# Optimization experiments

Measured on AMD Instinct MI355X. Metric: run time of the kernel, lower is better.

## Reference

```python
import jax, jax.numpy as jnp
import numpy as np

D_MODEL = 1024
N_HEADS = 16
HEAD_DIM = D_MODEL // N_HEADS
D_FF = 4 * D_MODEL
LN_EPS = 1e-5


def setup_inputs() -> dict:
    key = jax.random.key(0)
    ks = jax.random.split(key, 12)
    B, T = 16, 512
    s = lambda fan_in: 1.0 / np.sqrt(fan_in)
    inp = {
        'x': jax.random.normal(ks[0], (B, T, D_MODEL), jnp.float32),
        # torch Linear layout: [out_features, in_features]
        'w_qkv': jax.random.normal(ks[1], (3 * D_MODEL, D_MODEL), jnp.float32) * s(D_MODEL),
        'w_proj': jax.random.normal(ks[2], (D_MODEL, D_MODEL), jnp.float32) * s(D_MODEL),
        'w_ff1': jax.random.normal(ks[3], (D_FF, D_MODEL), jnp.float32) * s(D_MODEL),
        'b_ff1': jax.random.normal(ks[4], (D_FF,), jnp.float32) * 0.02,
        'w_ff2': jax.random.normal(ks[5], (D_MODEL, D_FF), jnp.float32) * s(D_FF),
        'b_ff2': jax.random.normal(ks[6], (D_MODEL,), jnp.float32) * 0.02,
        'ln1_g': jnp.ones((D_MODEL,), jnp.float32),
        'ln1_b': jnp.zeros((D_MODEL,), jnp.float32),
        'ln2_g': jnp.ones((D_MODEL,), jnp.float32),
        'ln2_b': jnp.zeros((D_MODEL,), jnp.float32),
    }
    return inp


def _layernorm(x, g, b):
    mu = jnp.mean(x, axis=-1, keepdims=True)
    var = jnp.var(x, axis=-1, keepdims=True)
    return (x - mu) * jax.lax.rsqrt(var + LN_EPS) * g + b


def _block(x, w_qkv, w_proj, w_ff1, b_ff1, w_ff2, b_ff2, ln1_g, ln1_b, ln2_g, ln2_b):
    B, T, _ = x.shape
    a = _layernorm(x, ln1_g, ln1_b)
    qkv = a @ w_qkv.T  # [B,T,3D]
    q, k, v = jnp.split(qkv, 3, axis=-1)
    # [B,H,T,hd]
    rs = lambda t: t.reshape(B, T, N_HEADS, HEAD_DIM).transpose(0, 2, 1, 3)
    q, k, v = rs(q), rs(k), rs(v)
    scale = HEAD_DIM ** -0.5
    att = jnp.einsum('bhqd,bhkd->bhqk', q, k) * scale
    causal = jnp.tril(jnp.ones((T, T), bool))
    att = jnp.where(causal, att, jnp.float32(-10000.0))
    att = jax.nn.softmax(att, axis=-1)
    out = jnp.einsum('bhqk,bhkd->bhqd', att, v)
    out = out.transpose(0, 2, 1, 3).reshape(B, T, D_MODEL)
    x = x + out @ w_proj.T
    f = _layernorm(x, ln2_g, ln2_b)
    f = jax.nn.gelu(f @ w_ff1.T + b_ff1, approximate=False) @ w_ff2.T + b_ff2
    return x + f


def reference(x, w_qkv, w_proj, w_ff1, b_ff1, w_ff2, b_ff2, ln1_g, ln1_b, ln2_g, ln2_b):
    return _block(x, w_qkv, w_proj, w_ff1, b_ff1, w_ff2, b_ff2, ln1_g, ln1_b, ln2_g, ln2_b)
```

## Files before the change

kernel.cpp:

```cpp
#include <hip/hip_runtime.h>
#include <stdint.h>

typedef __bf16 bf16x8_t __attribute__((ext_vector_type(8)));
typedef float f32x4_t __attribute__((ext_vector_type(4)));

#define DEV __device__ __forceinline__

DEV unsigned short f2bf(float f) {
  union { float f; uint32_t u; } v; v.f = f;
  uint32_t r = v.u + 0x7FFFu + ((v.u >> 16) & 1u);
  return (unsigned short)(r >> 16);
}

DEV void gl_lds16(const void* g, void* l) {
  __builtin_amdgcn_global_load_lds(
      (const __attribute__((address_space(1))) void*)g,
      (__attribute__((address_space(3))) void*)l, 16, 0, 0);
}

DEV void barx() {
  asm volatile("" ::: "memory");
  __builtin_amdgcn_s_barrier();
  asm volatile("" ::: "memory");
}

#define VMC(N) asm volatile("s_waitcnt vmcnt(" #N ")" ::: "memory")

DEV float gelu_f(float x) {
  const float y = x * 0.7071067811865475f;
  const float ay = fabsf(y);
  const float t = __builtin_amdgcn_rcpf(1.0f + 0.3275911f * ay);
  float p = fmaf(t, 1.061405429f, -1.453152027f);
  p = fmaf(t, p, 1.421413741f);
  p = fmaf(t, p, -0.284496736f);
  p = fmaf(t, p, 0.254829592f);
  p *= t;
  const float e = __expf(-ay * ay);
  float erfv = 1.0f - p * e;
  erfv = copysignf(erfv, y);
  return 0.5f * x * (1.0f + erfv);
}

__global__ __launch_bounds__(256) void cvt_all(const float* __restrict__ w0, unsigned short* __restrict__ o0,
                                               const float* __restrict__ w1, unsigned short* __restrict__ o1,
                                               const float* __restrict__ w2, unsigned short* __restrict__ o2,
                                               const float* __restrict__ w3, unsigned short* __restrict__ o3) {
  int i = blockIdx.x * 256 + threadIdx.x;
  const float* in; unsigned short* outp;
  if (i < 786432) { in = w0; outp = o0; }
  else if (i < 1048576) { in = w1; outp = o1; i -= 786432; }
  else if (i < 2097152) { in = w2; outp = o2; i -= 1048576; }
  else { in = w3; outp = o3; i -= 2097152; }
  float4 v = ((const float4*)in)[i];
  ushort4 o;
  o.x = f2bf(v.x); o.y = f2bf(v.y); o.z = f2bf(v.z); o.w = f2bf(v.w);
  ((ushort4*)outp)[i] = o;
}

__global__ __launch_bounds__(256) void ln_kernel(const float* __restrict__ x,
                                                 const float* __restrict__ g,
                                                 const float* __restrict__ b,
                                                 unsigned short* __restrict__ outp) {
  const int row = blockIdx.x * 4 + (threadIdx.x >> 6);
  const int lane = threadIdx.x & 63;
  const float4* xr = (const float4*)(x + (size_t)row * 1024);
  float4 v[4];
  float s = 0.f, s2 = 0.f;
#pragma unroll
  for (int j = 0; j < 4; ++j) {
    v[j] = xr[j * 64 + lane];
    s += v[j].x + v[j].y + v[j].z + v[j].w;
    s2 += v[j].x * v[j].x + v[j].y * v[j].y + v[j].z * v[j].z + v[j].w * v[j].w;
  }
#pragma unroll
  for (int off = 1; off < 64; off <<= 1) {
    s += __shfl_xor(s, off, 64);
    s2 += __shfl_xor(s2, off, 64);
  }
  const float mu = s * (1.0f / 1024.0f);
  const float var = s2 * (1.0f / 1024.0f) - mu * mu;
  const float rstd = rsqrtf(var + 1e-5f);
  ushort4* orow = (ushort4*)(outp + (size_t)row * 1024);
  const float4* gp = (const float4*)g;
  const float4* bp = (const float4*)b;
#pragma unroll
  for (int j = 0; j < 4; ++j) {
    float4 gv = gp[j * 64 + lane], bv = bp[j * 64 + lane];
    ushort4 o;
    o.x = f2bf((v[j].x - mu) * rstd * gv.x + bv.x);
    o.y = f2bf((v[j].y - mu) * rstd * gv.y + bv.y);
    o.z = f2bf((v[j].z - mu) * rstd * gv.z + bv.z);
    o.w = f2bf((v[j].w - mu) * rstd * gv.w + bv.w);
    orow[j * 64 + lane] = o;
  }
}


#define RD_AF(DST, BUF, MH, PC)                                               \
  _Pragma("unroll") for (int mi = 0; mi < 4; ++mi)                            \
      DST[mi] = *(const bf16x8_t*)((BUF) + (wm + (MH)*64 + mi * 16 + l16) * 64 + (PC));

#define RD_BF(DST, BUF, PC)                                                   \
  _Pragma("unroll") for (int ni = 0; ni < 4; ++ni)                            \
      DST[ni] = *(const bf16x8_t*)((BUF) + (wn + ni * 16 + l16) * 64 + (PC));

#define MFMA16(MH, AA, BB)                                                    \
  __builtin_amdgcn_s_setprio(1);                                              \
  _Pragma("unroll") for (int mi = 0; mi < 4; ++mi)                            \
  _Pragma("unroll") for (int ni = 0; ni < 4; ++ni)                            \
      acc[(MH)*4 + mi][ni] = __builtin_amdgcn_mfma_f32_16x16x32_bf16(         \
          AA[mi], BB[ni], acc[(MH)*4 + mi][ni], 0, 0, 0);                     \
  __builtin_amdgcn_s_setprio(0);

#define DMA_A(BUF, Q, KT) gl_lds16(aBase + (size_t)((Q)*64) * lda + (size_t)(KT)*64, &sA[BUF][(Q)*4096 + sdo])
#define DMA_B(BUF, Q, KT) gl_lds16(bBase + (size_t)((Q)*64) * lda + (size_t)(KT)*64, &sB[BUF][(Q)*4096 + sdo])

#define TILE(T, CB, B0c, B1c, B0n)                                            \
  {                                                                           \
    const int t1 = ((T) + 1 < nt) ? (T) + 1 : nt - 1;                         \
    const int t2 = ((T) + 2 < nt) ? (T) + 2 : nt - 1;                         \
    const unsigned short* pA = &sA[CB][0];                                    \
    const unsigned short* pB = &sB[CB][0];                                    \
                                                                     \
    barx(); VMC(8);                                                           \
    RD_AF(aO, pA, 0, pc1) RD_BF(B1c, pB, pc1)                                 \
    MFMA16(0, aE, B0c)                                                        \
    DMA_A(CB ^ 1, 1, t1); DMA_A(CB ^ 1, 3, t1);                               \
                                                                     \
    barx(); VMC(8);                                                           \
    RD_AF(aE, pA, 1, pc0)                                                     \
    MFMA16(0, aO, B1c)                                                        \
    DMA_B(CB, 0, t2); DMA_B(CB, 1, t2);                                       \
                                                                     \
    barx();                                                                   \
    RD_AF(aO, pA, 1, pc1)                                                     \
    MFMA16(1, aE, B0c)                                                        \
    DMA_A(CB, 0, t2); DMA_A(CB, 2, t2);                                       \
                                                                     \
    barx(); VMC(6);                                                           \
    RD_AF(aE, &sA[CB ^ 1][0], 0, pc0) RD_BF(B0n, &sB[CB ^ 1][0], pc0)         \
    MFMA16(1, aO, B1c)                                                        \
    DMA_B(CB, 2, t2); DMA_B(CB, 3, t2);                                       \
  }

template <int MODE>
__global__ __launch_bounds__(512) void gemm8(const unsigned short* __restrict__ A,
                                             const unsigned short* __restrict__ B,
                                             float* __restrict__ Cf,
                                             unsigned short* __restrict__ Cb,
                                             const float* __restrict__ bias,
                                             const float* __restrict__ res,
                                             unsigned short* __restrict__ Vt,
                                             int M, int N, int K, int lda) {
  __shared__ unsigned short sA[2][256 * 64];
  __shared__ unsigned short sB[2][256 * 64];
  const int tid = threadIdx.x;
  const int w = tid >> 6, lane = tid & 63;
  const int kg = lane >> 4, l16 = lane & 15;
  const int wm = (w & 1) * 128, wn = (w >> 1) * 64;

  const int nwg = gridDim.x;
  const int bid = blockIdx.x;
  const int cid = (bid & 7) * (nwg >> 3) + (bid >> 3);
  int ks = 0, cc = cid;
  if (MODE == 4) { ks = cid >> 7; cc = cid & 127; }
  const int rowBase = (cc & 31) * 256;
  const int colBase = (cc >> 5) * 256;
  const int koff = ks * K;

  const int srow = tid >> 3, sch = tid & 7;
  const unsigned short* aBase = A + (size_t)(rowBase + srow) * lda + koff + ((sch ^ (srow & 7)) * 8);
  const unsigned short* bBase = B + (size_t)(colBase + srow) * lda + koff + ((sch ^ (srow & 7)) * 8);
  const int sdo = tid * 8;

  f32x4_t acc[8][4];
#pragma unroll
  for (int mi = 0; mi < 8; ++mi)
#pragma unroll
    for (int ni = 0; ni < 4; ++ni) acc[mi][ni] = (f32x4_t)0.0f;

  const int nt = K >> 6;
  const int pc0 = ((kg ^ (l16 & 7)) & 7) * 8;
  const int pc1 = (((4 + kg) ^ (l16 & 7)) & 7) * 8;

  bf16x8_t aE[4], aO[4], B0a[4], B1a[4], B0b[4], B1b[4];

  {
    const int t1p = 1 < nt ? 1 : 0;
#pragma unroll
    for (int q = 0; q < 4; ++q) DMA_A(0, q, 0);
#pragma unroll
    for (int q = 0; q < 4; ++q) DMA_B(0, q, 0);
    DMA_A(1, 0, t1p); DMA_A(1, 2, t1p);
#pragma unroll
    for (int q = 0; q < 4; ++q) DMA_B(1, q, t1p);
  }
  VMC(6);
  barx();
  RD_AF(aE, &sA[0][0], 0, pc0)
  RD_BF(B0a, &sB[0][0], pc0)

  for (int t = 0; t < nt; t += 2) {
    TILE(t, 0, B0a, B1a, B0b)
    TILE(t + 1, 1, B0b, B1b, B0a)
  }

#pragma unroll
  for (int mi = 0; mi < 8; ++mi) {
#pragma unroll
    for (int ni = 0; ni < 4; ++ni) {
      const int col = colBase + wn + ni * 16 + l16;
      if (MODE == 0 && colBase >= 2048) {
        const int c2 = col - 2048;
        const int hh = c2 >> 6, dd = c2 & 63;
        const int rw = rowBase + wm + mi * 16 + kg * 4;
        ushort4 pk;
        pk.x = f2bf(acc[mi][ni][0]);
        pk.y = f2bf(acc[mi][ni][1]);
        pk.z = f2bf(acc[mi][ni][2]);
        pk.w = f2bf(acc[mi][ni][3]);
        *(ushort4*)(Vt + (((size_t)(rw >> 9) * 16 + hh) * 64 + dd) * 512 + (rw & 511)) = pk;
        continue;
      }
      float bv = 0.f;
      if (MODE == 2 || MODE == 3 || (MODE == 4 && ks == 0)) bv = bias[col];
#pragma unroll
      for (int r = 0; r < 4; ++r) {
        const int row = rowBase + wm + mi * 16 + kg * 4 + r;
        const size_t idx = (size_t)row * N + col;
        float v = acc[mi][ni][r];
        if (MODE == 0) {
          Cb[idx] = f2bf(v);
        } else if (MODE == 1) {
          Cf[idx] = v + res[idx];
        } else if (MODE == 2) {
          Cb[idx] = f2bf(gelu_f(v + bv));
        } else if (MODE == 3) {
          Cf[idx] = v + bv + res[idx];
        } else {
          if (ks == 0) {
            Cf[idx] = v + bv + res[idx];
          } else {
            float* P = (rowBase < 4096) ? (float*)Cb : (float*)Vt;
            P[(size_t)((row & 4095)) * N + col] = v;
          }
        }
      }
    }
  }
  asm volatile("s_waitcnt vmcnt(0)" ::: "memory");
}

__global__ __launch_bounds__(256) void ff2_fin(float* __restrict__ outp,
                                               const float* __restrict__ p1a,
                                               const float* __restrict__ p1b) {
  const int i = blockIdx.x * 256 + threadIdx.x;
  float4 v = ((float4*)outp)[i];
  const float4 p = (i < 1048576) ? ((const float4*)p1a)[i] : ((const float4*)p1b)[i - 1048576];
  v.x += p.x; v.y += p.y; v.z += p.z; v.w += p.w;
  ((float4*)outp)[i] = v;
}

__global__ __launch_bounds__(256) void attn_kernel(const unsigned short* __restrict__ qkv,
                                                   const unsigned short* __restrict__ Vt,
                                                   unsigned short* __restrict__ outp) {
  constexpr int D3 = 3072;
  __shared__ unsigned short sQ[128 * 64];
  __shared__ unsigned short sK[64 * 64];
  __shared__ unsigned short sVt[64 * 64];
  __shared__ unsigned short sP[128 * 72];
  const int tid = threadIdx.x;
  const int w = tid >> 6, lane = tid & 63;
  const int kg = lane >> 4, l16 = lane & 15;
  const int qi = (int)gridDim.x - 1 - (int)blockIdx.x;
  const int h = blockIdx.y, bb = blockIdx.z;
  const int t0 = qi * 128;
  const size_t base = (size_t)bb * 512 * D3 + h * 64;

  const int sr = tid >> 3;
  const int sc = ((tid & 7) ^ (sr & 7)) * 8;

  {
    const unsigned short* g = qkv + base + (size_t)(t0 + sr) * D3 + sc;
    unsigned short* l = sQ + tid * 8;
#pragma unroll
    for (int i = 0; i < 4; ++i) gl_lds16(g + (size_t)32 * i * D3, l + 2048 * i);
  }

  const unsigned short* gVbase = Vt + ((size_t)(bb * 16 + h) * 64 + sr) * 512 + sc;

  bf16x8_t ones;
#pragma unroll
  for (int j = 0; j < 8; ++j) ones[j] = (__bf16)1.0f;

  const int wm = w * 32;
  f32x4_t o[2][4];
  f32x4_t lsum[2];
#pragma unroll
  for (int mi = 0; mi < 2; ++mi) {
    lsum[mi] = (f32x4_t)0.0f;
#pragma unroll
    for (int di = 0; di < 4; ++di) o[mi][di] = (f32x4_t)0.0f;
  }

  const int nkt = (qi + 1) * 2;
  for (int kt = 0; kt < nkt; ++kt) {
    const int k0 = kt * 64;
    __syncthreads();
    {
      const unsigned short* g = qkv + base + 1024 + (size_t)(k0 + sr) * D3 + sc;
      unsigned short* l = sK + tid * 8;
      gl_lds16(g, l);
      gl_lds16(g + (size_t)32 * D3, l + 2048);
    }
    {
      const unsigned short* g = gVbase + k0;
      unsigned short* l = sVt + tid * 8;
      gl_lds16(g, l);
      gl_lds16(g + (size_t)32 * 512, l + 2048);
    }
    __syncthreads();

    const bool active = (k0 <= t0 + wm + 31);
    if (active) {
      f32x4_t s[2][4];
#pragma unroll
      for (int mi = 0; mi < 2; ++mi)
#pragma unroll
        for (int ni = 0; ni < 4; ++ni) s[mi][ni] = (f32x4_t)0.0f;
#pragma unroll
      for (int kd = 0; kd < 2; ++kd) {
        bf16x8_t aq[2], bk[4];
#pragma unroll
        for (int mi = 0; mi < 2; ++mi) {
          const int rr = wm + mi * 16 + l16;
          aq[mi] = *(const bf16x8_t*)(sQ + rr * 64 + (((kd * 4 + kg) ^ (l16 & 7)) * 8));
        }
#pragma unroll
        for (int ni = 0; ni < 4; ++ni) {
          const int rr = ni * 16 + l16;
          bk[ni] = *(const bf16x8_t*)(sK + rr * 64 + (((kd * 4 + kg) ^ (l16 & 7)) * 8));
        }
#pragma unroll
        for (int mi = 0; mi < 2; ++mi)
#pragma unroll
          for (int ni = 0; ni < 4; ++ni)
            s[mi][ni] = __builtin_amdgcn_mfma_f32_16x16x32_bf16(aq[mi], bk[ni], s[mi][ni], 0, 0, 0);
      }
#pragma unroll
      for (int mi = 0; mi < 2; ++mi) {
#pragma unroll
        for (int r = 0; r < 4; ++r) {
          const int q = t0 + wm + mi * 16 + kg * 4 + r;
          const int prow = wm + mi * 16 + kg * 4 + r;
#pragma unroll
          for (int ni = 0; ni < 4; ++ni) {
            const int kk = k0 + ni * 16 + l16;
            const float p = (kk <= q) ? __expf(s[mi][ni][r] * 0.125f) : 0.0f;
            sP[prow * 72 + ni * 16 + l16] = f2bf(p);
          }
        }
      }
#pragma unroll
      for (int kd = 0; kd < 2; ++kd) {
        bf16x8_t ap[2], bv[4];
#pragma unroll
        for (int mi = 0; mi < 2; ++mi)
          ap[mi] = *(const bf16x8_t*)(sP + (wm + mi * 16 + l16) * 72 + kd * 32 + kg * 8);
#pragma unroll
        for (int di = 0; di < 4; ++di) {
          const int dd = di * 16 + l16;
          bv[di] = *(const bf16x8_t*)(sVt + dd * 64 + (((kd * 4 + kg) ^ (l16 & 7)) * 8));
        }
#pragma unroll
        for (int mi = 0; mi < 2; ++mi) {
#pragma unroll
          for (int di = 0; di < 4; ++di)
            o[mi][di] = __builtin_amdgcn_mfma_f32_16x16x32_bf16(ap[mi], bv[di], o[mi][di], 0, 0, 0);
          lsum[mi] = __builtin_amdgcn_mfma_f32_16x16x32_bf16(ap[mi], ones, lsum[mi], 0, 0, 0);
        }
      }
    }
  }

#pragma unroll
  for (int mi = 0; mi < 2; ++mi) {
#pragma unroll
    for (int r = 0; r < 4; ++r) {
      const float inv = 1.0f / lsum[mi][r];
      const int row = t0 + wm + mi * 16 + kg * 4 + r;
      const size_t ob = ((size_t)bb * 512 + row) * 1024 + h * 64;
#pragma unroll
      for (int di = 0; di < 4; ++di)
        outp[ob + di * 16 + l16] = f2bf(o[mi][di][r] * inv);
    }
  }
}

extern "C" void kernel_launch(void* const* d_in, const int* in_sizes, int n_in,
                              void* d_out, int out_size, void* d_ws, size_t ws_size,
                              hipStream_t stream) {
  const float* x      = (const float*)d_in[0];
  const float* w_qkv  = (const float*)d_in[1];
  const float* w_proj = (const float*)d_in[2];
  const float* w_ff1  = (const float*)d_in[3];
  const float* b_ff1  = (const float*)d_in[4];
  const float* w_ff2  = (const float*)d_in[5];
  const float* b_ff2  = (const float*)d_in[6];
  const float* ln1_g  = (const float*)d_in[7];
  const float* ln1_b  = (const float*)d_in[8];
  const float* ln2_g  = (const float*)d_in[9];
  const float* ln2_b  = (const float*)d_in[10];
  float* out = (float*)d_out;
  char* ws = (char*)d_ws;

  unsigned short* wqkv_b  = (unsigned short*)(ws + 0);
  unsigned short* wproj_b = (unsigned short*)(ws + 6291456);
  unsigned short* wff1_b  = (unsigned short*)(ws + 8388608);
  unsigned short* wff2_b  = (unsigned short*)(ws + 16777216);
  unsigned short* a_b     = (unsigned short*)(ws + 25165824);
  float*          x2_f    = (float*)(ws + 41943040);
  unsigned short* vt_b    = (unsigned short*)(ws + 41943040);
  unsigned short* qkv_b   = (unsigned short*)(ws + 75497472);
  unsigned short* attn_b  = (unsigned short*)(ws + 125829120);
  unsigned short* h_b     = qkv_b;
  float* p1a = (float*)a_b;
  float* p1b = (float*)attn_b;

  cvt_all<<<12288, 256, 0, stream>>>(w_qkv, wqkv_b, w_proj, wproj_b, w_ff1, wff1_b, w_ff2, wff2_b);

  ln_kernel<<<2048, 256, 0, stream>>>(x, ln1_g, ln1_b, a_b);
  gemm8<0><<<384, 512, 0, stream>>>(a_b, wqkv_b, nullptr, qkv_b, nullptr, nullptr, vt_b, 8192, 3072, 1024, 1024);
  attn_kernel<<<dim3(4, 16, 16), 256, 0, stream>>>(qkv_b, vt_b, attn_b);
  gemm8<1><<<128, 512, 0, stream>>>(attn_b, wproj_b, x2_f, nullptr, nullptr, x, nullptr, 8192, 1024, 1024, 1024);
  ln_kernel<<<2048, 256, 0, stream>>>(x2_f, ln2_g, ln2_b, a_b);
  gemm8<2><<<512, 512, 0, stream>>>(a_b, wff1_b, nullptr, h_b, b_ff1, nullptr, nullptr, 8192, 4096, 1024, 1024);
  gemm8<4><<<256, 512, 0, stream>>>(h_b, wff2_b, out, (unsigned short*)p1a, b_ff2, x2_f, (unsigned short*)p1b, 8192, 1024, 2048, 4096);
  ff2_fin<<<8192, 256, 0, stream>>>(out, p1a, p1b);
}
```

Measured before the change: 484.9 us.

## Restructure GEMM main loop into per-k-tile four-phase schedule with simpler buffering

Replaces the two-tile unrolled TILE macro pipeline, which prefetched A/B fragments into registers across tiles, with a single k-tile loop split into four phases. Each phase reads a 32-row A slice plus the full B fragment set from LDS, issues part of the next tile's DMA, waits on lgkmcnt, and runs the MFMAs. Register pressure and fragment ping-ponging drop, but there are more barriers and no LDS-read/MFMA overlap across phases, since each phase waits with lgkmcnt(0) before its MFMAs.

Measured after the change: 525.4 us. +8.4%, slower.

```diff
diff --git a/kernel.cpp b/kernel.cpp
--- a/kernel.cpp
+++ b/kernel.cpp
@@ -25,6 +25,11 @@
 }
 
 #define VMC(N) asm volatile("s_waitcnt vmcnt(" #N ")" ::: "memory")
+#define LGKM(N) asm volatile("s_waitcnt lgkmcnt(" #N ")" ::: "memory")
+
+DEV f32x4_t mfma(bf16x8_t a, bf16x8_t b, f32x4_t c) {
+  return __builtin_amdgcn_mfma_f32_16x16x32_bf16(a, b, c, 0, 0, 0);
+}
 
 DEV float gelu_f(float x) {
   const float y = x * 0.7071067811865475f;
@@ -96,52 +101,30 @@
 }
 
 
-#define RD_AF(DST, BUF, MH, PC)                                               \
-  _Pragma("unroll") for (int mi = 0; mi < 4; ++mi)                            \
-      DST[mi] = *(const bf16x8_t*)((BUF) + (wm + (MH)*64 + mi * 16 + l16) * 64 + (PC));
-
-#define RD_BF(DST, BUF, PC)                                                   \
-  _Pragma("unroll") for (int ni = 0; ni < 4; ++ni)                            \
-      DST[ni] = *(const bf16x8_t*)((BUF) + (wn + ni * 16 + l16) * 64 + (PC));
-
-#define MFMA16(MH, AA, BB)                                                    \
+#define RD_A4(Q, BUF)                                                         \
+  aF[0] = *(const bf16x8_t*)((BUF) + (wm + (Q)*32 + l16) * 64 + pc0);         \
+  aF[1] = *(const bf16x8_t*)((BUF) + (wm + (Q)*32 + l16) * 64 + pc1);         \
+  aF[2] = *(const bf16x8_t*)((BUF) + (wm + (Q)*32 + 16 + l16) * 64 + pc0);    \
+  aF[3] = *(const bf16x8_t*)((BUF) + (wm + (Q)*32 + 16 + l16) * 64 + pc1);
+
+#define RD_B8(BUF)                                                            \
+  _Pragma("unroll") for (int ni = 0; ni < 4; ++ni) {                          \
+    bF[ni] = *(const bf16x8_t*)((BUF) + (wn + ni * 16 + l16) * 64 + pc0);     \
+    bF[4 + ni] = *(const bf16x8_t*)((BUF) + (wn + ni * 16 + l16) * 64 + pc1); \
+  }
+
+#define MFMA_Q(Q)                                                             \
   __builtin_amdgcn_s_setprio(1);                                              \
-  _Pragma("unroll") for (int mi = 0; mi < 4; ++mi)                            \
-  _Pragma("unroll") for (int ni = 0; ni < 4; ++ni)                            \
-      acc[(MH)*4 + mi][ni] = __builtin_amdgcn_mfma_f32_16x16x32_bf16(         \
-          AA[mi], BB[ni], acc[(MH)*4 + mi][ni], 0, 0, 0);                     \
+  _Pragma("unroll") for (int ni = 0; ni < 4; ++ni) {                          \
+    acc[(Q)*2][ni] = mfma(aF[0], bF[ni], acc[(Q)*2][ni]);                     \
+    acc[(Q)*2][ni] = mfma(aF[1], bF[4 + ni], acc[(Q)*2][ni]);                 \
+    acc[(Q)*2 + 1][ni] = mfma(aF[2], bF[ni], acc[(Q)*2 + 1][ni]);             \
+    acc[(Q)*2 + 1][ni] = mfma(aF[3], bF[4 + ni], acc[(Q)*2 + 1][ni]);         \
+  }                                                                           \
   __builtin_amdgcn_s_setprio(0);
 
 #define DMA_A(BUF, Q, KT) gl_lds16(aBase + (size_t)((Q)*64) * lda + (size_t)(KT)*64, &sA[BUF][(Q)*4096 + sdo])
 #define DMA_B(BUF, Q, KT) gl_lds16(bBase + (size_t)((Q)*64) * lda + (size_t)(KT)*64, &sB[BUF][(Q)*4096 + sdo])
-
-#define TILE(T, CB, B0c, B1c, B0n)                                            \
-  {                                                                           \
-    const int t1 = ((T) + 1 < nt) ? (T) + 1 : nt - 1;                         \
-    const int t2 = ((T) + 2 < nt) ? (T) + 2 : nt - 1;                         \
-    const unsigned short* pA = &sA[CB][0];                                    \
-    const unsigned short* pB = &sB[CB][0];                                    \
-                                                                     \
-    barx(); VMC(8);                                                           \
-    RD_AF(aO, pA, 0, pc1) RD_BF(B1c, pB, pc1)                                 \
-    MFMA16(0, aE, B0c)                                                        \
-    DMA_A(CB ^ 1, 1, t1); DMA_A(CB ^ 1, 3, t1);                               \
-                                                                     \
-    barx(); VMC(8);                                                           \
-    RD_AF(aE, pA, 1, pc0)                                                     \
-    MFMA16(0, aO, B1c)                                                        \
-    DMA_B(CB, 0, t2); DMA_B(CB, 1, t2);                                       \
-                                                                     \
-    barx();                                                                   \
-    RD_AF(aO, pA, 1, pc1)                                                     \
-    MFMA16(1, aE, B0c)                                                        \
-    DMA_A(CB, 0, t2); DMA_A(CB, 2, t2);                                       \
-                                                                     \
-    barx(); VMC(6);                                                           \
-    RD_AF(aE, &sA[CB ^ 1][0], 0, pc0) RD_BF(B0n, &sB[CB ^ 1][0], pc0)         \
-    MFMA16(1, aO, B1c)                                                        \
-    DMA_B(CB, 2, t2); DMA_B(CB, 3, t2);                                       \
-  }
 
 template <int MODE>
 __global__ __launch_bounds__(512) void gemm8(const unsigned short* __restrict__ A,
@@ -183,26 +166,51 @@
   const int pc0 = ((kg ^ (l16 & 7)) & 7) * 8;
   const int pc1 = (((4 + kg) ^ (l16 & 7)) & 7) * 8;
 
-  bf16x8_t aE[4], aO[4], B0a[4], B1a[4], B0b[4], B1b[4];
-
-  {
-    const int t1p = 1 < nt ? 1 : 0;
-#pragma unroll
-    for (int q = 0; q < 4; ++q) DMA_A(0, q, 0);
-#pragma unroll
-    for (int q = 0; q < 4; ++q) DMA_B(0, q, 0);
-    DMA_A(1, 0, t1p); DMA_A(1, 2, t1p);
-#pragma unroll
-    for (int q = 0; q < 4; ++q) DMA_B(1, q, t1p);
-  }
-  VMC(6);
+  DMA_A(0, 0, 0); DMA_A(0, 2, 0);
+  DMA_B(0, 0, 0); DMA_B(0, 1, 0); DMA_B(0, 2, 0); DMA_B(0, 3, 0);
+  DMA_A(0, 1, 0); DMA_A(0, 3, 0);
+  VMC(2);
   barx();
-  RD_AF(aE, &sA[0][0], 0, pc0)
-  RD_BF(B0a, &sB[0][0], pc0)
-
-  for (int t = 0; t < nt; t += 2) {
-    TILE(t, 0, B0a, B1a, B0b)
-    TILE(t + 1, 1, B0b, B1b, B0a)
+
+  for (int kt = 0; kt < nt; ++kt) {
+    const int cur = kt & 1;
+    const unsigned short* pA = &sA[cur][0];
+    const unsigned short* pB = &sB[cur][0];
+    const int nb = cur ^ 1;
+    const int t1 = (kt + 1 < nt) ? kt + 1 : nt - 1;
+    bf16x8_t aF[4], bF[8];
+
+    RD_A4(0, pA)
+    RD_B8(pB)
+    DMA_A(nb, 0, t1); DMA_A(nb, 2, t1);
+    LGKM(8);
+    barx();
+    LGKM(0);
+    MFMA_Q(0)
+    barx();
+
+    RD_A4(1, pA)
+    DMA_B(nb, 0, t1); DMA_B(nb, 1, t1);
+    barx();
+    LGKM(0);
+    MFMA_Q(1)
+    VMC(4);
+    barx();
+
+    RD_A4(2, pA)
+    DMA_B(nb, 2, t1); DMA_B(nb, 3, t1);
+    barx();
+    LGKM(0);
+    MFMA_Q(2)
+    barx();
+
+    RD_A4(3, pA)
+    DMA_A(nb, 1, t1); DMA_A(nb, 3, t1);
+    barx();
+    LGKM(0);
+    MFMA_Q(3)
+    VMC(2);
+    barx();
   }
 
 #pragma unroll
```

## Replace big-tile GEMMs with smaller-tile kernel for QKV, proj and FF2; drop split-K

Applied to the files above, without the earlier changes.

Adds a simpler 256-thread GEMM with 128x128 or 64x128 tiles, a K-step of 32 and double-buffered LDS. It is used for the QKV, projection and FF2 GEMMs, while FF1 stays on the 256x256 kernel. FF2 no longer uses split-K with partial buffers and a separate reduction kernel; it now runs one full-K pass over more, smaller tiles. The aim is better CU occupancy and less extra traffic, but the new kernel has less data reuse and a shallower pipeline than the tuned 256x256 kernel.

Measured after the change: 473.3 us. 2.4% less time.

```diff
diff --git a/kernel.cpp b/kernel.cpp
--- a/kernel.cpp
+++ b/kernel.cpp
@@ -95,6 +95,114 @@
   }
 }
 
+template <int MODE, int BM>
+__global__ __launch_bounds__(256) void gemm_bt(const unsigned short* __restrict__ A,
+                                               const unsigned short* __restrict__ B,
+                                               float* __restrict__ Cf,
+                                               unsigned short* __restrict__ Cb,
+                                               const float* __restrict__ bias,
+                                               const float* __restrict__ res,
+                                               unsigned short* __restrict__ Vt,
+                                               int M, int N, int K) {
+  constexpr int MI = BM / 32;
+  constexpr int RT = 8192 / BM;
+  constexpr int ABUF = BM * 32;
+  __shared__ unsigned short sA[2][ABUF];
+  __shared__ unsigned short sB[2][128 * 32];
+  const int tid = threadIdx.x;
+  const int w = tid >> 6, lane = tid & 63;
+  const int kg = lane >> 4, l16 = lane & 15;
+  const int wm = (w & 1) * (BM / 2), wn = (w >> 1) * 64;
+
+  const int cid = blockIdx.y * gridDim.x + blockIdx.x;
+  const int colBase = (cid / RT) * 128;
+  const int rowBase = (cid % RT) * BM;
+
+  const int sr = (BM == 128) ? (tid >> 2) : ((tid >> 2) & 63);
+  const int gc = ((tid & 3) ^ ((sr >> 1) & 3)) * 8;
+  const unsigned short* gA = A + (size_t)(rowBase + sr) * K + gc;
+  const unsigned short* gB = B + (size_t)(colBase + sr) * K + gc;
+
+  f32x4_t acc[MI][4];
+#pragma unroll
+  for (int mi = 0; mi < MI; ++mi)
+#pragma unroll
+    for (int ni = 0; ni < 4; ++ni) acc[mi][ni] = (f32x4_t)0.0f;
+
+  int offA[MI], offB[4];
+  const int pc = (kg ^ ((l16 >> 1) & 3)) * 8;
+#pragma unroll
+  for (int i = 0; i < MI; ++i) offA[i] = (wm + i * 16 + l16) * 32 + pc;
+#pragma unroll
+  for (int i = 0; i < 4; ++i) offB[i] = (wn + i * 16 + l16) * 32 + pc;
+
+  gl_lds16(gA, &sA[0][tid * 8]);
+  if (BM == 128) gl_lds16(gA + (size_t)64 * K, &sA[0][2048 + tid * 8]);
+  gl_lds16(gB, &sB[0][tid * 8]);
+  gl_lds16(gB + (size_t)64 * K, &sB[0][2048 + tid * 8]);
+  gA += 32; gB += 32;
+
+  const int nk = K >> 5;
+  for (int kt = 0; kt < nk; ++kt) {
+    __syncthreads();
+    if (kt + 1 < nk) {
+      const int nb = (kt + 1) & 1;
+      gl_lds16(gA, &sA[nb][tid * 8]);
+      if (BM == 128) gl_lds16(gA + (size_t)64 * K, &sA[nb][2048 + tid * 8]);
+      gl_lds16(gB, &sB[nb][tid * 8]);
+      gl_lds16(gB + (size_t)64 * K, &sB[nb][2048 + tid * 8]);
+      gA += 32; gB += 32;
+    }
+    const int par = kt & 1;
+    bf16x8_t a[MI], b[4];
+#pragma unroll
+    for (int i = 0; i < MI; ++i) a[i] = *(const bf16x8_t*)(&sA[par][0] + offA[i]);
+#pragma unroll
+    for (int i = 0; i < 4; ++i) b[i] = *(const bf16x8_t*)(&sB[par][0] + offB[i]);
+#pragma unroll
+    for (int mi = 0; mi < MI; ++mi)
+#pragma unroll
+      for (int ni = 0; ni < 4; ++ni)
+        acc[mi][ni] = __builtin_amdgcn_mfma_f32_16x16x32_bf16(a[mi], b[ni], acc[mi][ni], 0, 0, 0);
+  }
+
+#pragma unroll
+  for (int mi = 0; mi < MI; ++mi) {
+#pragma unroll
+    for (int ni = 0; ni < 4; ++ni) {
+      const int col = colBase + wn + ni * 16 + l16;
+      if (MODE == 0 && colBase >= 2048) {
+        const int c2 = col - 2048;
+        const int hh = c2 >> 6, dd = c2 & 63;
+        const int rw = rowBase + wm + mi * 16 + kg * 4;
+        ushort4 pk;
+        pk.x = f2bf(acc[mi][ni][0]);
+        pk.y = f2bf(acc[mi][ni][1]);
+        pk.z = f2bf(acc[mi][ni][2]);
+        pk.w = f2bf(acc[mi][ni][3]);
+        *(ushort4*)(Vt + (((size_t)(rw >> 9) * 16 + hh) * 64 + dd) * 512 + (rw & 511)) = pk;
+        continue;
+      }
+      float bv = 0.f;
+      if (MODE == 2 || MODE == 3) bv = bias[col];
+#pragma unroll
+      for (int r = 0; r < 4; ++r) {
+        const int row = rowBase + wm + mi * 16 + kg * 4 + r;
+        const size_t idx = (size_t)row * N + col;
+        float v = acc[mi][ni][r];
+        if (MODE == 0) {
+          Cb[idx] = f2bf(v);
+        } else if (MODE == 1) {
+          Cf[idx] = v + res[idx];
+        } else if (MODE == 2) {
+          Cb[idx] = f2bf(gelu_f(v + bv));
+        } else {
+          Cf[idx] = v + bv + res[idx];
+        }
+      }
+    }
+  }
+}
 
 #define RD_AF(DST, BUF, MH, PC)                                               \
   _Pragma("unroll") for (int mi = 0; mi < 4; ++mi)                            \
@@ -162,15 +270,12 @@
   const int nwg = gridDim.x;
   const int bid = blockIdx.x;
   const int cid = (bid & 7) * (nwg >> 3) + (bid >> 3);
-  int ks = 0, cc = cid;
-  if (MODE == 4) { ks = cid >> 7; cc = cid & 127; }
-  const int rowBase = (cc & 31) * 256;
-  const int colBase = (cc >> 5) * 256;
-  const int koff = ks * K;
+  const int rowBase = (cid & 31) * 256;
+  const int colBase = (cid >> 5) * 256;
 
   const int srow = tid >> 3, sch = tid & 7;
-  const unsigned short* aBase = A + (size_t)(rowBase + srow) * lda + koff + ((sch ^ (srow & 7)) * 8);
-  const unsigned short* bBase = B + (size_t)(colBase + srow) * lda + koff + ((sch ^ (srow & 7)) * 8);
+  const unsigned short* aBase = A + (size_t)(rowBase + srow) * lda + ((sch ^ (srow & 7)) * 8);
+  const unsigned short* bBase = B + (size_t)(colBase + srow) * lda + ((sch ^ (srow & 7)) * 8);
   const int sdo = tid * 8;
 
   f32x4_t acc[8][4];
@@ -210,20 +315,8 @@
 #pragma unroll
     for (int ni = 0; ni < 4; ++ni) {
       const int col = colBase + wn + ni * 16 + l16;
-      if (MODE == 0 && colBase >= 2048) {
-        const int c2 = col - 2048;
-        const int hh = c2 >> 6, dd = c2 & 63;
-        const int rw = rowBase + wm + mi * 16 + kg * 4;
-        ushort4 pk;
-        pk.x = f2bf(acc[mi][ni][0]);
-        pk.y = f2bf(acc[mi][ni][1]);
-        pk.z = f2bf(acc[mi][ni][2]);
-        pk.w = f2bf(acc[mi][ni][3]);
-        *(ushort4*)(Vt + (((size_t)(rw >> 9) * 16 + hh) * 64 + dd) * 512 + (rw & 511)) = pk;
-        continue;
-      }
       float bv = 0.f;
-      if (MODE == 2 || MODE == 3 || (MODE == 4 && ks == 0)) bv = bias[col];
+      if (MODE == 2 || MODE == 3) bv = bias[col];
 #pragma unroll
       for (int r = 0; r < 4; ++r) {
         const int row = rowBase + wm + mi * 16 + kg * 4 + r;
@@ -235,30 +328,13 @@
           Cf[idx] = v + res[idx];
         } else if (MODE == 2) {
           Cb[idx] = f2bf(gelu_f(v + bv));
-        } else if (MODE == 3) {
+        } else {
           Cf[idx] = v + bv + res[idx];
-        } else {
-          if (ks == 0) {
-            Cf[idx] = v + bv + res[idx];
-          } else {
-            float* P = (rowBase < 4096) ? (float*)Cb : (float*)Vt;
-            P[(size_t)((row & 4095)) * N + col] = v;
-          }
         }
       }
     }
   }
   asm volatile("s_waitcnt vmcnt(0)" ::: "memory");
-}
-
-__global__ __launch_bounds__(256) void ff2_fin(float* __restrict__ outp,
-                                               const float* __restrict__ p1a,
-                                               const float* __restrict__ p1b) {
-  const int i = blockIdx.x * 256 + threadIdx.x;
-  float4 v = ((float4*)outp)[i];
-  const float4 p = (i < 1048576) ? ((const float4*)p1a)[i] : ((const float4*)p1b)[i - 1048576];
-  v.x += p.x; v.y += p.y; v.z += p.z; v.w += p.w;
-  ((float4*)outp)[i] = v;
 }
 
 __global__ __launch_bounds__(256) void attn_kernel(const unsigned short* __restrict__ qkv,
@@ -424,17 +500,14 @@
   unsigned short* qkv_b   = (unsigned short*)(ws + 75497472);
   unsigned short* attn_b  = (unsigned short*)(ws + 125829120);
   unsigned short* h_b     = qkv_b;
-  float* p1a = (float*)a_b;
-  float* p1b = (float*)attn_b;
 
   cvt_all<<<12288, 256, 0, stream>>>(w_qkv, wqkv_b, w_proj, wproj_b, w_ff1, wff1_b, w_ff2, wff2_b);
 
   ln_kernel<<<2048, 256, 0, stream>>>(x, ln1_g, ln1_b, a_b);
-  gemm8<0><<<384, 512, 0, stream>>>(a_b, wqkv_b, nullptr, qkv_b, nullptr, nullptr, vt_b, 8192, 3072, 1024, 1024);
+  gemm_bt<0, 128><<<dim3(24, 64), 256, 0, stream>>>(a_b, wqkv_b, nullptr, qkv_b, nullptr, nullptr, vt_b, 8192, 3072, 1024);
   attn_kernel<<<dim3(4, 16, 16), 256, 0, stream>>>(qkv_b, vt_b, attn_b);
-  gemm8<1><<<128, 512, 0, stream>>>(attn_b, wproj_b, x2_f, nullptr, nullptr, x, nullptr, 8192, 1024, 1024, 1024);
+  gemm_bt<1, 64><<<dim3(8, 128), 256, 0, stream>>>(attn_b, wproj_b, x2_f, nullptr, nullptr, x, nullptr, 8192, 1024, 1024);
   ln_kernel<<<2048, 256, 0, stream>>>(x2_f, ln2_g, ln2_b, a_b);
   gemm8<2><<<512, 512, 0, stream>>>(a_b, wff1_b, nullptr, h_b, b_ff1, nullptr, nullptr, 8192, 4096, 1024, 1024);
-  gemm8<4><<<256, 512, 0, stream>>>(h_b, wff2_b, out, (unsigned short*)p1a, b_ff2, x2_f, (unsigned short*)p1b, 8192, 1024, 2048, 4096);
-  ff2_fin<<<8192, 256, 0, stream>>>(out, p1a, p1b);
-}
+  gemm_bt<3, 64><<<dim3(8, 128), 256, 0, stream>>>(h_b, wff2_b, out, nullptr, b_ff2, x2_f, nullptr, 8192, 1024, 4096);
+}
```
